# Optimization experiments

Hardware: AMD Instinct MI355X
Metric: run time of the kernel (lower is better)

The kernel has to match this reference:

```python
import jax, jax.numpy as jnp
import numpy as np

N, E, D, H = 50000, 600000, 128, 8
C = D // H  # per-head channels

def _layernorm(x, g, b, eps=1e-5):
    mu = jnp.mean(x, axis=-1, keepdims=True)
    var = jnp.var(x, axis=-1, keepdims=True)
    return (x - mu) * jax.lax.rsqrt(var + eps) * g + b

def setup_inputs() -> dict:
    key = jax.random.key(0)
    ks = jax.random.split(key, 16)
    s = 0.02
    w = lambda k, shape: jax.random.normal(k, shape, jnp.float32) * s
    return {
        "x": jax.random.normal(ks[0], (N, D), jnp.float32),
        "edge_attr": jax.random.normal(ks[1], (E, D), jnp.float32),
        "edge_index": jax.random.randint(ks[2], (2, E), 0, N, jnp.int64),
        # TransformerConv params (PyG: lin_query/key/value with bias, lin_edge no bias, lin_skip root weight)
        "Wq": w(ks[3], (D, D)), "bq": jnp.zeros((D,), jnp.float32),
        "Wk": w(ks[4], (D, D)), "bk": jnp.zeros((D,), jnp.float32),
        "Wv": w(ks[5], (D, D)), "bv": jnp.zeros((D,), jnp.float32),
        "We": w(ks[6], (D, D)),
        "Wskip": w(ks[7], (D, D)), "bskip": jnp.zeros((D,), jnp.float32),
        # FFN
        "W1": w(ks[8], (D, 4 * D)), "b1": jnp.zeros((4 * D,), jnp.float32),
        "W2": w(ks[9], (4 * D, D)), "b2": jnp.zeros((D,), jnp.float32),
        # LayerNorms + residual scale
        "g1": jnp.ones((D,), jnp.float32), "beta1": jnp.zeros((D,), jnp.float32),
        "g2": jnp.ones((D,), jnp.float32), "beta2": jnp.zeros((D,), jnp.float32),
        "alpha": jnp.ones((1,), jnp.float32),
    }

def reference(x, edge_attr, edge_index, Wq, bq, Wk, bk, Wv, bv, We, Wskip, bskip,
              W1, b1, W2, b2, g1, beta1, g2, beta2, alpha):
    n = x.shape[0]
    src, dst = edge_index[0], edge_index[1]

    h = _layernorm(x, g1, beta1)

    # --- TransformerConv ---
    q = (h @ Wq + bq)[dst].reshape(-1, H, C)              # [E,H,C]
    e = (edge_attr @ We).reshape(-1, H, C)                # [E,H,C]
    k = (h @ Wk + bk)[src].reshape(-1, H, C) + e          # [E,H,C]
    v = (h @ Wv + bv)[src].reshape(-1, H, C) + e          # [E,H,C]

    logits = jnp.sum(q * k, axis=-1) / jnp.sqrt(jnp.float32(C))  # [E,H]
    # segment softmax over incoming edges per destination node
    m = jax.ops.segment_max(logits, dst, num_segments=n)          # [N,H]
    p = jnp.exp(logits - m[dst])                                   # [E,H]
    z = jax.ops.segment_sum(p, dst, num_segments=n)               # [N,H]
    attn = p / (z[dst] + 1e-16)                                    # [E,H]

    msg = attn[..., None] * v                                      # [E,H,C]
    out = jax.ops.segment_sum(msg, dst, num_segments=n).reshape(n, H * C)
    out = out + h @ Wskip + bskip                                  # root weight (skip)

    x = x + alpha * out

    h2 = _layernorm(x, g2, beta2)
    ffn = jax.nn.silu(h2 @ W1 + b1) @ W2 + b2
    return x + ffn
```

## Files before the change

kernel.cpp:

```cpp
#include <hip/hip_runtime.h>
#include <hip/hip_bf16.h>

typedef __bf16 bf16x8 __attribute__((ext_vector_type(8)));
typedef __bf16 bf16x4 __attribute__((ext_vector_type(4)));
typedef __bf16 bf16x2 __attribute__((ext_vector_type(2)));
typedef float f32x4 __attribute__((ext_vector_type(4)));
using bf16 = __hip_bfloat16;

__global__ __launch_bounds__(256) void t_k(const float* __restrict__ W,
                                           bf16* __restrict__ WT, int K, int N)
{
    int idx = blockIdx.x * 256 + threadIdx.x;
    if (idx >= K * N) return;
    int n = idx / K, k = idx % K;
    WT[idx] = __float2bfloat16(W[(size_t)k * N + n]);
}

__global__ __launch_bounds__(256) void bcat_k(const float* __restrict__ a, const float* __restrict__ b,
                                              const float* __restrict__ c, const float* __restrict__ d,
                                              float* __restrict__ o)
{
    int i = threadIdx.x + blockIdx.x * 256;
    if (i >= 512) return;
    o[i] = (i < 128) ? a[i] : (i < 256) ? b[i - 128] : (i < 384) ? c[i - 256] : d[i - 384];
}

template <int MODE, bool AF32>
__global__ __launch_bounds__(512) void gemm2_k(
    const void* __restrict__ Av, const bf16* __restrict__ WT,
    const float* __restrict__ bias, void* __restrict__ Cout,
    const float* __restrict__ resid, const int* __restrict__ rowperm,
    int M, int K, int Nout)
{
    __shared__ __bf16 As[128 * 128];
    __shared__ __bf16 Ws[128 * 128];

    const int tid  = threadIdx.x;
    const int wave = tid >> 6;
    const int lane = tid & 63;
    const int row0 = blockIdx.x * 128;
    const int col0 = blockIdx.y * 128;

    f32x4 acc[8];
#pragma unroll
    for (int i = 0; i < 8; i++) acc[i] = (f32x4){0.f, 0.f, 0.f, 0.f};

    for (int k0 = 0; k0 < K; k0 += 128) {
        if constexpr (AF32) {
            const float* A = (const float*)Av;
#pragma unroll
            for (int i = 0; i < 8; i++) {
                int idx = tid + i * 512;
                int r = idx >> 5, c4 = idx & 31;
                bf16x4 o;
                if (row0 + r < M) {
                    f32x4 v = *reinterpret_cast<const f32x4*>(A + (size_t)(row0 + r) * K + k0 + c4 * 4);
#pragma unroll
                    for (int j = 0; j < 4; j++) o[j] = (__bf16)v[j];
                } else {
#pragma unroll
                    for (int j = 0; j < 4; j++) o[j] = (__bf16)0.f;
                }
                int col = (c4 >> 1) ^ (r & 7);
                *reinterpret_cast<bf16x4*>(&As[r * 128 + col * 8 + (c4 & 1) * 4]) = o;
            }
        } else {
            const bf16* A = (const bf16*)Av;
#pragma unroll
            for (int i = 0; i < 4; i++) {
                int idx = tid + i * 512;
                int r = idx >> 4, c = idx & 15;
                bf16x8 v;
                if (row0 + r < M) {
                    v = *reinterpret_cast<const bf16x8*>(A + (size_t)(row0 + r) * K + k0 + c * 8);
                } else {
#pragma unroll
                    for (int j = 0; j < 8; j++) v[j] = (__bf16)0.f;
                }
                *reinterpret_cast<bf16x8*>(&As[r * 128 + ((c ^ (r & 7)) * 8)]) = v;
            }
        }
#pragma unroll
        for (int i = 0; i < 4; i++) {
            int idx = tid + i * 512;
            int r = idx >> 4, c = idx & 15;
            bf16x8 v = *reinterpret_cast<const bf16x8*>(WT + (size_t)(col0 + r) * K + k0 + c * 8);
            *reinterpret_cast<bf16x8*>(&Ws[r * 128 + ((c ^ (r & 7)) * 8)]) = v;
        }
        __syncthreads();

        const int mrow = wave * 16 + (lane & 15);
        const int kq = lane >> 4;
#pragma unroll
        for (int kk = 0; kk < 4; kk++) {
            int cidx = kk * 4 + kq;
            bf16x8 a = *reinterpret_cast<const bf16x8*>(&As[mrow * 128 + ((cidx ^ (mrow & 7)) * 8)]);
#pragma unroll
            for (int ct = 0; ct < 8; ct++) {
                int nrow = ct * 16 + (lane & 15);
                bf16x8 b = *reinterpret_cast<const bf16x8*>(&Ws[nrow * 128 + ((cidx ^ (nrow & 7)) * 8)]);
                acc[ct] = __builtin_amdgcn_mfma_f32_16x16x32_bf16(a, b, acc[ct], 0, 0, 0);
            }
        }
        __syncthreads();
    }

    const int rbase = row0 + wave * 16 + ((lane >> 4) << 2);
    int orow[4];
#pragma unroll
    for (int r = 0; r < 4; r++) {
        int row = rbase + r;
        orow[r] = (row < M) ? (rowperm ? rowperm[row] : row) : -1;
    }
#pragma unroll
    for (int ct = 0; ct < 8; ct++) {
        int col = col0 + ct * 16 + (lane & 15);
        float bv = bias ? bias[col] : 0.f;
#pragma unroll
        for (int r = 0; r < 4; r++) {
            if (orow[r] < 0) continue;
            float v = acc[ct][r] + bv;
            if constexpr (MODE == 2) v = v / (1.f + __expf(-v));
            if constexpr (MODE == 3) v += resid[(size_t)orow[r] * 128 + col];
            if constexpr (MODE == 3) {
                ((float*)Cout)[(size_t)orow[r] * Nout + col] = v;
            } else {
                ((bf16*)Cout)[(size_t)orow[r] * Nout + col] = __float2bfloat16(v);
            }
        }
    }
}

__global__ __launch_bounds__(256) void ln_k(
    const float* __restrict__ x, const float* __restrict__ g,
    const float* __restrict__ beta, bf16* __restrict__ h, int Nrows)
{
    int row = blockIdx.x * 4 + (threadIdx.x >> 6);
    int lane = threadIdx.x & 63;
    if (row >= Nrows) return;
    size_t base = (size_t)row * 128;
    float v0 = x[base + lane], v1 = x[base + lane + 64];
    float s = v0 + v1, ss = v0 * v0 + v1 * v1;
#pragma unroll
    for (int off = 32; off; off >>= 1) {
        s += __shfl_xor(s, off, 64);
        ss += __shfl_xor(ss, off, 64);
    }
    float mu = s * (1.f / 128.f);
    float var = ss * (1.f / 128.f) - mu * mu;
    float rs = rsqrtf(var + 1e-5f);
    h[base + lane]      = __float2bfloat16((v0 - mu) * rs * g[lane] + beta[lane]);
    h[base + lane + 64] = __float2bfloat16((v1 - mu) * rs * g[lane + 64] + beta[lane + 64]);
}

__global__ __launch_bounds__(256) void hist_k(const int* __restrict__ ei, int* __restrict__ cnt, int E)
{
    int e = blockIdx.x * 256 + threadIdx.x;
    if (e < E) atomicAdd(&cnt[ei[E + e]], 1);
}

__global__ __launch_bounds__(1024) void scan_k(const int* __restrict__ cnt, int* __restrict__ offset, int N)
{
    __shared__ int tmp[1024];
    __shared__ int s_running;
    int tid = threadIdx.x;
    if (tid == 0) { s_running = 0; offset[0] = 0; }
    __syncthreads();
    for (int base = 0; base < N; base += 1024) {
        int v = (base + tid < N) ? cnt[base + tid] : 0;
        tmp[tid] = v;
        __syncthreads();
#pragma unroll
        for (int off = 1; off < 1024; off <<= 1) {
            int t = (tid >= off) ? tmp[tid - off] : 0;
            __syncthreads();
            tmp[tid] += t;
            __syncthreads();
        }
        int run = s_running;
        if (base + tid < N) offset[base + tid + 1] = run + tmp[tid];
        __syncthreads();
        if (tid == 0) s_running = run + tmp[1023];
        __syncthreads();
    }
}

__global__ __launch_bounds__(256) void scatter_k(
    const int* __restrict__ ei, const int* __restrict__ offset,
    int* __restrict__ cursor, int* __restrict__ srcs, int* __restrict__ epos, int E)
{
    int e = blockIdx.x * 256 + threadIdx.x;
    if (e >= E) return;
    int src = ei[e];
    int dst = ei[E + e];
    int r = atomicAdd(&cursor[dst], 1);
    int j = offset[dst] + r;
    srcs[j] = src;
    epos[e] = j;
}

__global__ __launch_bounds__(256) void gather_k(
    const int* __restrict__ srcs, const int* __restrict__ offset,
    const bf16* __restrict__ QKVS, const bf16* __restrict__ Ep,
    const float* __restrict__ x, const float* __restrict__ alpha,
    const float* __restrict__ g, const float* __restrict__ beta,
    float* __restrict__ xn, bf16* __restrict__ h2, int N)
{
    int node = blockIdx.x * 4 + (threadIdx.x >> 6);
    if (node >= N) return;
    int lane = threadIdx.x & 63;
    int c = lane * 2;

    bf16x2 qv = *reinterpret_cast<const bf16x2*>(QKVS + (size_t)node * 512 + c);
    float q0 = (float)qv[0], q1 = (float)qv[1];

    int start = offset[node], end = offset[node + 1];
    float den = 0.f, num0 = 0.f, num1 = 0.f;

    bf16x2 kv, vv, ev;
    if (start < end) {
        const bf16* sp = QKVS + (size_t)srcs[start] * 512 + c;
        kv = *reinterpret_cast<const bf16x2*>(sp + 128);
        vv = *reinterpret_cast<const bf16x2*>(sp + 256);
        ev = *reinterpret_cast<const bf16x2*>(Ep + (size_t)start * 128 + c);
    }
    for (int j = start; j < end; j++) {
        bf16x2 kc = kv, vc = vv, ec = ev;
        if (j + 1 < end) {
            const bf16* sp = QKVS + (size_t)srcs[j + 1] * 512 + c;
            kv = *reinterpret_cast<const bf16x2*>(sp + 128);
            vv = *reinterpret_cast<const bf16x2*>(sp + 256);
            ev = *reinterpret_cast<const bf16x2*>(Ep + (size_t)(j + 1) * 128 + c);
        }
        float e0 = (float)ec[0], e1 = (float)ec[1];
        float part = q0 * ((float)kc[0] + e0) + q1 * ((float)kc[1] + e1);
        part += __shfl_xor(part, 1, 64);
        part += __shfl_xor(part, 2, 64);
        part += __shfl_xor(part, 4, 64);
        float p = __expf(part * 0.25f);
        den  += p;
        num0 += p * ((float)vc[0] + e0);
        num1 += p * ((float)vc[1] + e1);
    }

    size_t base = (size_t)node * 128;
    float invz = 1.f / (den + 1e-16f);
    float al = alpha[0];
    float s0 = (float)QKVS[(size_t)node * 512 + 384 + c];
    float s1 = (float)QKVS[(size_t)node * 512 + 384 + c + 1];
    float o0 = num0 * invz + s0;
    float o1 = num1 * invz + s1;
    float x0 = x[base + c] + al * o0;
    float x1 = x[base + c + 1] + al * o1;
    xn[base + c] = x0;
    xn[base + c + 1] = x1;

    float s = x0 + x1, ss = x0 * x0 + x1 * x1;
#pragma unroll
    for (int off = 32; off; off >>= 1) {
        s += __shfl_xor(s, off, 64);
        ss += __shfl_xor(ss, off, 64);
    }
    float mu = s * (1.f / 128.f);
    float var = ss * (1.f / 128.f) - mu * mu;
    float rs = rsqrtf(var + 1e-5f);
    h2[base + c]     = __float2bfloat16((x0 - mu) * rs * g[c] + beta[c]);
    h2[base + c + 1] = __float2bfloat16((x1 - mu) * rs * g[c + 1] + beta[c + 1]);
}

extern "C" void kernel_launch(void* const* d_in, const int* in_sizes, int n_in,
                              void* d_out, int out_size, void* d_ws, size_t ws_size,
                              hipStream_t stream)
{
    const float* x         = (const float*)d_in[0];
    const float* edge_attr = (const float*)d_in[1];
    const int*   ei        = (const int*)d_in[2];
    const float* Wq = (const float*)d_in[3];  const float* bq = (const float*)d_in[4];
    const float* Wk = (const float*)d_in[5];  const float* bk = (const float*)d_in[6];
    const float* Wv = (const float*)d_in[7];  const float* bv = (const float*)d_in[8];
    const float* We = (const float*)d_in[9];
    const float* Wskip = (const float*)d_in[10]; const float* bskip = (const float*)d_in[11];
    const float* W1 = (const float*)d_in[12]; const float* b1 = (const float*)d_in[13];
    const float* W2 = (const float*)d_in[14]; const float* b2 = (const float*)d_in[15];
    const float* g1 = (const float*)d_in[16]; const float* beta1 = (const float*)d_in[17];
    const float* g2 = (const float*)d_in[18]; const float* beta2 = (const float*)d_in[19];
    const float* alpha = (const float*)d_in[20];

    const int N = in_sizes[0] / 128;
    const int E = in_sizes[2] / 2;

    char* w = (char*)d_ws;
    auto alloc = [&](size_t bytes) {
        char* p = w;
        w += (bytes + 255) & ~(size_t)255;
        return p;
    };
    bf16*  h      = (bf16*)alloc((size_t)N * 128 * 2);
    bf16*  QKVS   = (bf16*)alloc((size_t)N * 512 * 2);
    bf16*  Ep     = (bf16*)alloc((size_t)E * 128 * 2);
    float* xn     = (float*)alloc((size_t)N * 128 * 4);
    bf16*  h2     = (bf16*)alloc((size_t)N * 128 * 2);
    bf16*  t      = (bf16*)alloc((size_t)N * 512 * 2);
    int*   cnt    = (int*)alloc((size_t)N * 4);
    int*   cursor = (int*)alloc((size_t)N * 4);
    int*   offset = (int*)alloc((size_t)(N + 1) * 4);
    int*   srcs   = (int*)alloc((size_t)E * 4);
    int*   epos   = (int*)alloc((size_t)E * 4);
    bf16*  WTqkvs = (bf16*)alloc((size_t)512 * 128 * 2);
    bf16*  WTe    = (bf16*)alloc((size_t)128 * 128 * 2);
    bf16*  WT1    = (bf16*)alloc((size_t)512 * 128 * 2);
    bf16*  WT2    = (bf16*)alloc((size_t)128 * 512 * 2);
    float* bqkvs  = (float*)alloc((size_t)512 * 4);

    t_k<<<64, 256, 0, stream>>>(Wq, WTqkvs, 128, 128);
    t_k<<<64, 256, 0, stream>>>(Wk, WTqkvs + 128 * 128, 128, 128);
    t_k<<<64, 256, 0, stream>>>(Wv, WTqkvs + 256 * 128, 128, 128);
    t_k<<<64, 256, 0, stream>>>(Wskip, WTqkvs + 384 * 128, 128, 128);
    t_k<<<64, 256, 0, stream>>>(We, WTe, 128, 128);
    t_k<<<256, 256, 0, stream>>>(W1, WT1, 128, 512);
    t_k<<<256, 256, 0, stream>>>(W2, WT2, 512, 128);
    bcat_k<<<2, 256, 0, stream>>>(bq, bk, bv, bskip, bqkvs);

    hipMemsetAsync(cnt, 0, (size_t)N * 4, stream);
    hipMemsetAsync(cursor, 0, (size_t)N * 4, stream);
    hist_k<<<(E + 255) / 256, 256, 0, stream>>>(ei, cnt, E);
    scan_k<<<1, 1024, 0, stream>>>(cnt, offset, N);
    scatter_k<<<(E + 255) / 256, 256, 0, stream>>>(ei, offset, cursor, srcs, epos, E);

    ln_k<<<(N + 3) / 4, 256, 0, stream>>>(x, g1, beta1, h, N);

    gemm2_k<0, false><<<dim3((N + 127) / 128, 4), 512, 0, stream>>>(h, WTqkvs, bqkvs, QKVS, nullptr, nullptr, N, 128, 512);

    gemm2_k<0, true><<<dim3((E + 127) / 128, 1), 512, 0, stream>>>(edge_attr, WTe, nullptr, Ep, nullptr, epos, E, 128, 128);

    gather_k<<<(N + 3) / 4, 256, 0, stream>>>(srcs, offset, QKVS, Ep, x, alpha, g2, beta2, xn, h2, N);

    gemm2_k<2, false><<<dim3((N + 127) / 128, 4), 512, 0, stream>>>(h2, WT1, b1, t, nullptr, nullptr, N, 128, 512);
    gemm2_k<3, false><<<dim3((N + 127) / 128, 1), 512, 0, stream>>>(t, WT2, b2, d_out, xn, nullptr, N, 512, 128);
}
```

Measured before the change: 944.2 us.

## Add persistent edge GEMM kernel with shared-memory resident weight and direct fp32 A loads

Replaces the generic tiled GEMM for the edge_attr @ We projection with a specialized persistent kernel. It loads the whole 128x128 bf16 weight once per block into XOR-swizzled shared memory, then has each wave loop over 16-row tiles. Each wave reads fp32 rows straight from global memory, converts them to bf16 in registers and runs MFMA 16x16x32. The aim is to remove per-tile A staging through LDS and repeated weight loads on this bandwidth-bound E=600k GEMM. Output stores are scalar bf16 writes to permuted rows, which may be poorly coalesced.

```diff
diff --git a/kernel.cpp b/kernel.cpp
--- a/kernel.cpp
+++ b/kernel.cpp
@@ -126,6 +126,78 @@
                 ((float*)Cout)[(size_t)orow[r] * Nout + col] = v;
             } else {
                 ((bf16*)Cout)[(size_t)orow[r] * Nout + col] = __float2bfloat16(v);
+            }
+        }
+    }
+}
+
+__global__ __launch_bounds__(256) void egemm_k(
+    const float* __restrict__ A, const bf16* __restrict__ WT,
+    bf16* __restrict__ C, const int* __restrict__ rowperm, int M)
+{
+    __shared__ __bf16 Ws[128 * 128];
+#pragma unroll
+    for (int i = 0; i < 8; i++) {
+        int idx = threadIdx.x + i * 256;
+        int r = idx >> 4, c = idx & 15;
+        bf16x8 v = *reinterpret_cast<const bf16x8*>(WT + r * 128 + c * 8);
+        *reinterpret_cast<bf16x8*>(&Ws[r * 128 + ((c ^ (r & 7)) * 8)]) = v;
+    }
+    __syncthreads();
+
+    const int lane = threadIdx.x & 63;
+    const int wave = threadIdx.x >> 6;
+    const int r16  = lane & 15;
+    const int kq   = lane >> 4;
+    const int ntiles = (M + 15) >> 4;
+
+    for (int t = blockIdx.x * 4 + wave; t < ntiles; t += gridDim.x * 4) {
+        const int row0 = t * 16;
+        const int arow = row0 + r16;
+
+        bf16x8 a[4];
+        if (arow < M) {
+            const float* ap = A + (size_t)arow * 128 + kq * 8;
+#pragma unroll
+            for (int kk = 0; kk < 4; kk++) {
+                f32x4 lo = *reinterpret_cast<const f32x4*>(ap + kk * 32);
+                f32x4 hi = *reinterpret_cast<const f32x4*>(ap + kk * 32 + 4);
+#pragma unroll
+                for (int j = 0; j < 4; j++) {
+                    a[kk][j]     = (__bf16)lo[j];
+                    a[kk][j + 4] = (__bf16)hi[j];
+                }
+            }
+        } else {
+#pragma unroll
+            for (int kk = 0; kk < 4; kk++)
+#pragma unroll
+                for (int j = 0; j < 8; j++) a[kk][j] = (__bf16)0.f;
+        }
+
+        f32x4 acc[8];
+#pragma unroll
+        for (int i = 0; i < 8; i++) acc[i] = (f32x4){0.f, 0.f, 0.f, 0.f};
+#pragma unroll
+        for (int kk = 0; kk < 4; kk++) {
+            int cidx = kk * 4 + kq;
+#pragma unroll
+            for (int ct = 0; ct < 8; ct++) {
+                int nrow = ct * 16 + r16;
+                bf16x8 b = *reinterpret_cast<const bf16x8*>(&Ws[nrow * 128 + ((cidx ^ (nrow & 7)) * 8)]);
+                acc[ct] = __builtin_amdgcn_mfma_f32_16x16x32_bf16(a[kk], b, acc[ct], 0, 0, 0);
+            }
+        }
+
+        const int rbase = row0 + (kq << 2);
+#pragma unroll
+        for (int r = 0; r < 4; r++) {
+            int row = rbase + r;
+            if (row >= M) continue;
+            size_t orow = (size_t)(rowperm ? rowperm[row] : row);
+#pragma unroll
+            for (int ct = 0; ct < 8; ct++) {
+                C[orow * 128 + ct * 16 + r16] = __float2bfloat16(acc[ct][r]);
             }
         }
     }
@@ -331,7 +403,7 @@
 
     gemm2_k<0, false><<<dim3((N + 127) / 128, 4), 512, 0, stream>>>(h, WTqkvs, bqkvs, QKVS, nullptr, nullptr, N, 128, 512);
 
-    gemm2_k<0, true><<<dim3((E + 127) / 128, 1), 512, 0, stream>>>(edge_attr, WTe, nullptr, Ep, nullptr, epos, E, 128, 128);
+    egemm_k<<<1280, 256, 0, stream>>>(edge_attr, WTe, Ep, epos, E);
 
     gather_k<<<(N + 3) / 4, 256, 0, stream>>>(srcs, offset, QKVS, Ep, x, alpha, g2, beta2, xn, h2, N);
 
```

Result: faster. 903.5 us (-4.3%).
